# Kernel optimization log

Hardware: AMD Instinct MI355X
Metric: run time of the kernel (lower is better)

## Reference

```python
import jax, jax.numpy as jnp
import numpy as np

HIDDEN = 1152
N_HEADS = 4
N_KV = 1
HEAD_DIM = 256
EPS = 1e-6
B, S = 4, 2048
ROPE_THETA = 1000000.0


def _rms_norm(x, w):
    # x: [..., D] float32; Gemma-style (1 + w) scale
    xf = x.astype(jnp.float32)
    inv = jax.lax.rsqrt(jnp.mean(xf * xf, axis=-1, keepdims=True) + EPS)
    return (xf * inv * (1.0 + w.astype(jnp.float32))).astype(x.dtype)


def _apply_rope(x, cos, sin):
    # x: [B, H, S, D]; cos/sin: [S, D/2]
    d2 = x.shape[-1] // 2
    x1, x2 = x[..., :d2], x[..., d2:]
    cos = cos[None, None, :, :]
    sin = sin[None, None, :, :]
    xr = x1 * cos - x2 * sin
    xi = x1 * sin + x2 * cos
    return jnp.concatenate([xr, xi], axis=-1).astype(x.dtype)


def setup_inputs() -> dict:
    key = jax.random.key(0)
    k_h, k_qkv, k_qn, k_kn, k_o = jax.random.split(key, 5)
    hidden_states = jax.random.normal(k_h, (B, S, HIDDEN), dtype=jnp.float32)
    # causal additive mask [1,1,S,S]
    neg = jnp.finfo(jnp.float32).min
    causal = jnp.tril(jnp.ones((S, S), dtype=bool))
    attention_mask = jnp.where(causal, 0.0, neg)[None, None, :, :].astype(jnp.float32)
    # RoPE tables (complex freqs_cis split into cos/sin)
    inv_freq = 1.0 / (ROPE_THETA ** (np.arange(0, HEAD_DIM, 2, dtype=np.float32) / HEAD_DIM))
    ang = np.arange(S, dtype=np.float32)[:, None] * inv_freq[None, :]
    freqs_cos = jnp.asarray(np.cos(ang))
    freqs_sin = jnp.asarray(np.sin(ang))
    qkv_out = (N_HEADS + 2 * N_KV) * HEAD_DIM
    scale = HIDDEN ** -0.5
    w_qkv = jax.random.normal(k_qkv, (HIDDEN, qkv_out), dtype=jnp.float32) * scale
    w_o = jax.random.normal(k_o, (N_HEADS * HEAD_DIM, HIDDEN), dtype=jnp.float32) * (N_HEADS * HEAD_DIM) ** -0.5
    q_norm_w = jax.random.normal(k_qn, (HEAD_DIM,), dtype=jnp.float32) * 0.02
    k_norm_w = jax.random.normal(k_kn, (HEAD_DIM,), dtype=jnp.float32) * 0.02
    return {
        "hidden_states": hidden_states,
        "attention_mask": attention_mask,
        "freqs_cos": freqs_cos,
        "freqs_sin": freqs_sin,
        "w_qkv": w_qkv,
        "q_norm_w": q_norm_w,
        "k_norm_w": k_norm_w,
        "w_o": w_o,
    }


def reference(hidden_states, attention_mask, freqs_cos, freqs_sin, w_qkv, q_norm_w, k_norm_w, w_o):
    b, s, _ = hidden_states.shape
    groups = N_HEADS // N_KV
    scaling = HEAD_DIM ** -0.5

    qkv = jnp.einsum("bsh,ho->bso", hidden_states, w_qkv)
    q_end = N_HEADS * HEAD_DIM
    k_end = q_end + N_KV * HEAD_DIM
    q = qkv[:, :, :q_end].reshape(b, s, N_HEADS, HEAD_DIM).transpose(0, 2, 1, 3)
    k = qkv[:, :, q_end:k_end].reshape(b, s, N_KV, HEAD_DIM).transpose(0, 2, 1, 3)
    v = qkv[:, :, k_end:].reshape(b, s, N_KV, HEAD_DIM).transpose(0, 2, 1, 3)

    q = _rms_norm(q, q_norm_w)
    k = _rms_norm(k, k_norm_w)

    q = _apply_rope(q, freqs_cos, freqs_sin)
    k = _apply_rope(k, freqs_cos, freqs_sin)

    if groups > 1:
        k = jnp.repeat(k, groups, axis=1)  # [B, H, S, D]
        v = jnp.repeat(v, groups, axis=1)

    scores = jnp.einsum("bhqd,bhkd->bhqk", q * scaling, k)
    scores = scores + attention_mask.astype(jnp.float32)
    probs = jax.nn.softmax(scores.astype(jnp.float32), axis=-1).astype(q.dtype)

    attn = jnp.einsum("bhqk,bhkd->bhqd", probs, v)
    attn = attn.transpose(0, 2, 1, 3).reshape(b, s, N_HEADS * HEAD_DIM)
    return jnp.einsum("bsf,fh->bsh", attn, w_o)
```

## Files before the change

kernel.cpp:

```cpp
#include <hip/hip_runtime.h>

typedef _Float16 f16;
typedef _Float16 f16x8 __attribute__((ext_vector_type(8)));
typedef _Float16 f16x4 __attribute__((ext_vector_type(4)));
typedef float f32x4 __attribute__((ext_vector_type(4)));

#define NH 4
#define HD 256
#define BB 4
#define SS 2048
#define HID 1152
#define QKV_N 1536
#define ODIM (NH * HD)

#define QKV16_OFF 0L
#define HID16_OFF 25165824L
#define OBUF_OFF 0L
#define OPART_OFF 33554432L
#define QB_OFF 50331648L
#define KB_OFF 67108864L
#define VT_OFF 71303168L
#define WQKVT_OFF 75497472L
#define WOT_OFF 79036416L
#define ML_OFF 81395712L

#define GLL16(gp, lp)                                                      \
  __builtin_amdgcn_global_load_lds(                                       \
      (const __attribute__((address_space(1))) char*)(gp),                \
      (__attribute__((address_space(3))) char*)(lp), 16, 0, 0)

__global__ __launch_bounds__(256) void cvt_f32_to_f16(
    const float* __restrict__ s, f16* __restrict__ d, long n) {
  long i = ((long)blockIdx.x * 256 + threadIdx.x) * 8;
  long stride = (long)gridDim.x * 256 * 8;
  for (; i < n; i += stride) {
    float4 a = *(const float4*)(s + i);
    float4 b = *(const float4*)(s + i + 4);
    f16x8 h = {(f16)a.x, (f16)a.y, (f16)a.z, (f16)a.w,
               (f16)b.x, (f16)b.y, (f16)b.z, (f16)b.w};
    *(f16x8*)(d + i) = h;
  }
}

template <typename ST>
__global__ __launch_bounds__(256) void transpose_cvt(
    const ST* __restrict__ src, long src_ld, long src_bs,
    f16* __restrict__ dst, long dst_ld, long dst_bs) {
  __shared__ float tile[32][33];
  src += (long)blockIdx.z * src_bs;
  dst += (long)blockIdx.z * dst_bs;
  int r0 = blockIdx.y * 32, c0 = blockIdx.x * 32;
  int tc = threadIdx.x & 31, tr = threadIdx.x >> 5;
#pragma unroll
  for (int i = 0; i < 4; ++i)
    tile[tr + i * 8][tc] = (float)src[(long)(r0 + tr + i * 8) * src_ld + c0 + tc];
  __syncthreads();
#pragma unroll
  for (int i = 0; i < 4; ++i)
    dst[(long)(c0 + tr + i * 8) * dst_ld + r0 + tc] = (f16)tile[tc][tr + i * 8];
}

template <typename CT>
__global__ __launch_bounds__(256, 3) void gemm_f16(
    const f16* __restrict__ A, const f16* __restrict__ Bt,
    CT* __restrict__ C, int K, int N) {
  __shared__ f16 As[128][64];
  __shared__ f16 Bs[128][64];
  int tid = threadIdx.x, wave = tid >> 6, lane = tid & 63;
  int l16 = lane & 15, lhi = lane >> 4;
  int wm = (wave >> 1) * 64, wn = (wave & 1) * 64;
  long bm = (long)blockIdx.x * 128, bn = (long)blockIdx.y * 128;
  f32x4 acc[4][4] = {};

  int srow = wave * 32 + (lane >> 3);
  int scol = (lane & 7) * 8;
  const f16* Ag = A + (bm + srow) * (long)K + scol;
  const f16* Bg = Bt + (bn + srow) * (long)K + scol;

  for (int k0 = 0; k0 < K; k0 += 64) {
#pragma unroll
    for (int i = 0; i < 4; ++i)
      GLL16(Ag + k0 + (long)i * 8 * K, &As[wave * 32 + i * 8][0]);
#pragma unroll
    for (int i = 0; i < 4; ++i)
      GLL16(Bg + k0 + (long)i * 8 * K, &Bs[wave * 32 + i * 8][0]);
    __syncthreads();
#pragma unroll
    for (int kb = 0; kb < 2; ++kb) {
      f16x8 af[4], bf[4];
#pragma unroll
      for (int i = 0; i < 4; ++i)
        af[i] = *(const f16x8*)&As[wm + i * 16 + l16][kb * 32 + lhi * 8];
#pragma unroll
      for (int j = 0; j < 4; ++j)
        bf[j] = *(const f16x8*)&Bs[wn + j * 16 + l16][kb * 32 + lhi * 8];
#pragma unroll
      for (int i = 0; i < 4; ++i)
#pragma unroll
        for (int j = 0; j < 4; ++j)
          acc[i][j] =
              __builtin_amdgcn_mfma_f32_16x16x32_f16(bf[j], af[i], acc[i][j], 0, 0, 0);
    }
    __syncthreads();
  }

#pragma unroll
  for (int i = 0; i < 4; ++i) {
    long m = bm + wm + i * 16 + l16;
#pragma unroll
    for (int j = 0; j < 4; ++j) {
      long n = bn + wn + j * 16 + lhi * 4;
      if constexpr (sizeof(CT) == 2) {
        f16x4 h = {(f16)acc[i][j][0], (f16)acc[i][j][1], (f16)acc[i][j][2],
                   (f16)acc[i][j][3]};
        *(f16x4*)&C[m * N + n] = h;
      } else {
        *(f32x4*)&C[m * N + n] = acc[i][j];
      }
    }
  }
}

__device__ __forceinline__ void norm_rope_store(
    const f16* __restrict__ x, const float* __restrict__ w,
    const float* __restrict__ fc, const float* __restrict__ fs,
    f16* __restrict__ dst, float scale, int lane) {
  float x0 = (float)x[lane], x1 = (float)x[lane + 64];
  float x2 = (float)x[lane + 128], x3 = (float)x[lane + 192];
  float ss = x0 * x0 + x1 * x1 + x2 * x2 + x3 * x3;
#pragma unroll
  for (int m = 1; m < 64; m <<= 1) ss += __shfl_xor(ss, m, 64);
  float inv = rsqrtf(ss * (1.0f / 256.0f) + 1e-6f);
  x0 *= inv * (1.0f + w[lane]);
  x1 *= inv * (1.0f + w[lane + 64]);
  x2 *= inv * (1.0f + w[lane + 128]);
  x3 *= inv * (1.0f + w[lane + 192]);
  float c0 = fc[lane], s0 = fs[lane], c1 = fc[lane + 64], s1 = fs[lane + 64];
  dst[lane]       = (f16)((x0 * c0 - x2 * s0) * scale);
  dst[lane + 64]  = (f16)((x1 * c1 - x3 * s1) * scale);
  dst[lane + 128] = (f16)((x0 * s0 + x2 * c0) * scale);
  dst[lane + 192] = (f16)((x1 * s1 + x3 * c1) * scale);
}

__global__ __launch_bounds__(256) void qkv_post(
    const f16* __restrict__ qkv, const float* __restrict__ qnw,
    const float* __restrict__ knw, const float* __restrict__ fcos,
    const float* __restrict__ fsin, f16* __restrict__ Q, f16* __restrict__ Kb) {
  long row = blockIdx.x;
  int b = (int)(row >> 11), s = (int)(row & 2047);
  int wave = threadIdx.x >> 6, lane = threadIdx.x & 63;
  const f16* base = qkv + row * QKV_N;
  const float* fc = fcos + (long)s * 128;
  const float* fs = fsin + (long)s * 128;
  norm_rope_store(base + wave * HD, qnw, fc, fs,
                  Q + ((long)(b * NH + wave) * SS + s) * HD, 0.0625f, lane);
  if (wave == 0)
    norm_rope_store(base + NH * HD, knw, fc, fs, Kb + row * HD, 1.0f, lane);
}

__global__ __launch_bounds__(256, 3) void attn_fwd(
    const f16* __restrict__ Q, const f16* __restrict__ Kb,
    const f16* __restrict__ Vt, f16* __restrict__ O,
    f16* __restrict__ Opart, float2* __restrict__ ml) {
  __shared__ f16 Klds[32][264];
  __shared__ f16 Vlds[256][40];
  __shared__ f16 Plds[4][16][40];
  int it = blockIdx.x, h = blockIdx.y, b = blockIdx.z;
  int qb, t0, t1, pidx = 0;
  bool split;
  if (it < 16) {
    qb = it; t0 = 0; t1 = 2 * qb + 2; split = false;
  } else {
    int j = it - 16;
    qb = 16 + (j >> 1);
    int s = j & 1, half = qb + 1;
    t0 = s * half; t1 = t0 + half; split = true;
    pidx = (((b * NH + h) << 4) + (qb - 16)) * 2 + s;
  }
  int tid = threadIdx.x, wave = tid >> 6, lane = tid & 63;
  int l16 = lane & 15, lhi = lane >> 4;
  int q0 = qb * 64 + wave * 16;

  const f16* Kg = Kb + (long)b * SS * HD;
  const f16* Vg = Vt + (long)b * HD * SS;

  f16x8 qf[8];
  const f16* Qbase = Q + ((long)(b * NH + h) * SS + q0 + l16) * HD + lhi * 8;
#pragma unroll
  for (int kb = 0; kb < 8; ++kb) qf[kb] = *(const f16x8*)(Qbase + kb * 32);

  f32x4 o[16] = {};
  float m_i = -1e30f, l_i = 0.f;

  int kr = tid >> 5, kc = (tid & 31) * 8;
  int rv = tid >> 2, vc = (tid & 3) * 8;

  for (int t = t0; t < t1; ++t) {
    int kv0 = t * 32;
    __syncthreads();
#pragma unroll
    for (int i = 0; i < 4; ++i)
      *(uint4*)&Klds[kr + i * 8][kc] =
          *(const uint4*)(Kg + (long)(kv0 + kr + i * 8) * HD + kc);
#pragma unroll
    for (int i = 0; i < 4; ++i)
      *(uint4*)&Vlds[rv + i * 64][vc] =
          *(const uint4*)(Vg + (long)(rv + i * 64) * SS + kv0 + vc);
    __syncthreads();

    f32x4 sc[2] = {};
#pragma unroll
    for (int kb = 0; kb < 8; ++kb) {
#pragma unroll
      for (int cf = 0; cf < 2; ++cf) {
        f16x8 kf = *(const f16x8*)&Klds[cf * 16 + l16][kb * 32 + lhi * 8];
        sc[cf] = __builtin_amdgcn_mfma_f32_16x16x32_f16(kf, qf[kb], sc[cf], 0, 0, 0);
      }
    }

    float p[8];
    float mx = -1e30f;
    int qrow = q0 + l16;
    if (t >= 2 * qb) {
#pragma unroll
      for (int cf = 0; cf < 2; ++cf)
#pragma unroll
        for (int r = 0; r < 4; ++r) {
          int kv = kv0 + cf * 16 + lhi * 4 + r;
          float s = (kv <= qrow) ? sc[cf][r] : -1e30f;
          p[cf * 4 + r] = s;
          mx = fmaxf(mx, s);
        }
    } else {
#pragma unroll
      for (int i = 0; i < 8; ++i) {
        float s = sc[i >> 2][i & 3];
        p[i] = s;
        mx = fmaxf(mx, s);
      }
    }
    mx = fmaxf(mx, __shfl_xor(mx, 16));
    mx = fmaxf(mx, __shfl_xor(mx, 32));
    float mn = fmaxf(m_i, mx);
    float scl = __expf(m_i - mn);
    float rs = 0.f;
#pragma unroll
    for (int i = 0; i < 8; ++i) {
      p[i] = __expf(p[i] - mn);
      rs += p[i];
    }
    rs += __shfl_xor(rs, 16);
    rs += __shfl_xor(rs, 32);
    l_i = l_i * scl + rs;
    m_i = mn;

#pragma unroll
    for (int cf = 0; cf < 2; ++cf) {
      f16x4 hp = {(f16)p[cf * 4], (f16)p[cf * 4 + 1], (f16)p[cf * 4 + 2],
                  (f16)p[cf * 4 + 3]};
      *(f16x4*)&Plds[wave][l16][cf * 16 + lhi * 4] = hp;
    }

    float s0 = __shfl(scl, lhi * 4 + 0);
    float s1 = __shfl(scl, lhi * 4 + 1);
    float s2 = __shfl(scl, lhi * 4 + 2);
    float s3 = __shfl(scl, lhi * 4 + 3);
#pragma unroll
    for (int nf = 0; nf < 16; ++nf) {
      o[nf][0] *= s0;
      o[nf][1] *= s1;
      o[nf][2] *= s2;
      o[nf][3] *= s3;
    }

    f16x8 pa = *(const f16x8*)&Plds[wave][l16][lhi * 8];
#pragma unroll
    for (int nf = 0; nf < 16; ++nf) {
      f16x8 vf = *(const f16x8*)&Vlds[nf * 16 + l16][lhi * 8];
      o[nf] = __builtin_amdgcn_mfma_f32_16x16x32_f16(pa, vf, o[nf], 0, 0, 0);
    }
  }

  float inv = 1.0f / l_i;
  float i0 = __shfl(inv, lhi * 4 + 0);
  float i1 = __shfl(inv, lhi * 4 + 1);
  float i2 = __shfl(inv, lhi * 4 + 2);
  float i3 = __shfl(inv, lhi * 4 + 3);
  float ir[4] = {i0, i1, i2, i3};
  if (!split) {
#pragma unroll
    for (int r = 0; r < 4; ++r) {
      long srow = q0 + lhi * 4 + r;
      f16* Orow = O + ((long)b * SS + srow) * ODIM + h * HD + l16;
#pragma unroll
      for (int nf = 0; nf < 16; ++nf) Orow[nf * 16] = (f16)(o[nf][r] * ir[r]);
    }
  } else {
#pragma unroll
    for (int r = 0; r < 4; ++r) {
      int rloc = wave * 16 + lhi * 4 + r;
      f16* Prow = Opart + ((long)pidx * 64 + rloc) * HD + l16;
#pragma unroll
      for (int nf = 0; nf < 16; ++nf) Prow[nf * 16] = (f16)(o[nf][r] * ir[r]);
    }
    if (lane < 16) {
      float2 v; v.x = m_i; v.y = l_i;
      ml[(long)pidx * 64 + wave * 16 + lane] = v;
    }
  }
}

__global__ __launch_bounds__(256) void attn_combine(
    const f16* __restrict__ Opart, const float2* __restrict__ ml,
    f16* __restrict__ O) {
  int qx = blockIdx.x, h = blockIdx.y, b = blockIdx.z;
  int qb = 16 + qx;
  int p0 = (((b * NH + h) << 4) + qx) * 2;
  int tid = threadIdx.x;
  int r = tid >> 2, d0 = (tid & 3) * 64;
  float2 a = ml[(long)p0 * 64 + r];
  float2 c = ml[(long)(p0 + 1) * 64 + r];
  float M = fmaxf(a.x, c.x);
  float w0 = a.y * __expf(a.x - M), w1 = c.y * __expf(c.x - M);
  float invL = 1.0f / (w0 + w1);
  w0 *= invL; w1 *= invL;
  const f16* o0 = Opart + ((long)p0 * 64 + r) * HD + d0;
  const f16* o1 = Opart + ((long)(p0 + 1) * 64 + r) * HD + d0;
  f16* Orow = O + ((long)b * SS + qb * 64 + r) * ODIM + h * HD + d0;
#pragma unroll
  for (int i = 0; i < 8; ++i) {
    f16x8 x = *(const f16x8*)(o0 + i * 8);
    f16x8 y = *(const f16x8*)(o1 + i * 8);
    f16x8 z;
#pragma unroll
    for (int j = 0; j < 8; ++j)
      z[j] = (f16)(w0 * (float)x[j] + w1 * (float)y[j]);
    *(f16x8*)(Orow + i * 8) = z;
  }
}

extern "C" void kernel_launch(void* const* d_in, const int* in_sizes, int n_in,
                              void* d_out, int out_size, void* d_ws, size_t ws_size,
                              hipStream_t stream) {
  const float* hidden = (const float*)d_in[0];
  const float* fcos = (const float*)d_in[2];
  const float* fsin = (const float*)d_in[3];
  const float* wqkv = (const float*)d_in[4];
  const float* qnw = (const float*)d_in[5];
  const float* knw = (const float*)d_in[6];
  const float* wo = (const float*)d_in[7];
  float* out = (float*)d_out;

  char* ws = (char*)d_ws;
  f16* qkv16 = (f16*)(ws + QKV16_OFF);
  f16* hid16 = (f16*)(ws + HID16_OFF);
  f16* Obuf = (f16*)(ws + OBUF_OFF);
  f16* Opart = (f16*)(ws + OPART_OFF);
  f16* Qb = (f16*)(ws + QB_OFF);
  f16* Kb = (f16*)(ws + KB_OFF);
  f16* Vt = (f16*)(ws + VT_OFF);
  f16* wqkvt = (f16*)(ws + WQKVT_OFF);
  f16* wot = (f16*)(ws + WOT_OFF);
  float2* ml = (float2*)(ws + ML_OFF);

  cvt_f32_to_f16<<<2048, 256, 0, stream>>>(hidden, hid16, (long)BB * SS * HID);

  transpose_cvt<float><<<dim3(QKV_N / 32, HID / 32, 1), 256, 0, stream>>>(
      wqkv, QKV_N, 0, wqkvt, HID, 0);
  transpose_cvt<float><<<dim3(HID / 32, ODIM / 32, 1), 256, 0, stream>>>(
      wo, HID, 0, wot, ODIM, 0);

  gemm_f16<f16><<<dim3(BB * SS / 128, QKV_N / 128), 256, 0, stream>>>(
      hid16, wqkvt, qkv16, HID, QKV_N);

  qkv_post<<<dim3(BB * SS), 256, 0, stream>>>(qkv16, qnw, knw, fcos, fsin, Qb, Kb);

  transpose_cvt<f16><<<dim3(HD / 32, SS / 32, BB), 256, 0, stream>>>(
      qkv16 + 1280, QKV_N, (long)SS * QKV_N, Vt, SS, (long)HD * SS);

  attn_fwd<<<dim3(48, NH, BB), 256, 0, stream>>>(Qb, Kb, Vt, Obuf, Opart, ml);
  attn_combine<<<dim3(16, NH, BB), 256, 0, stream>>>(Opart, ml, Obuf);

  gemm_f16<float><<<dim3(BB * SS / 128, HID / 128), 256, 0, stream>>>(
      Obuf, wot, out, ODIM, HID);
}
```

Before: 237.0 us.

## Enlarge attention query tile to 128 rows with balanced causal pairing and K/V register prefetch

Measured after the change: 307.3 us. 29.7% more time.

```diff
diff --git a/kernel.cpp b/kernel.cpp
--- a/kernel.cpp
+++ b/kernel.cpp
@@ -158,154 +158,191 @@
     norm_rope_store(base + NH * HD, knw, fc, fs, Kb + row * HD, 1.0f, lane);
 }
 
-__global__ __launch_bounds__(256, 3) void attn_fwd(
+__global__ __launch_bounds__(256, 1) void attn_fwd(
     const f16* __restrict__ Q, const f16* __restrict__ Kb,
     const f16* __restrict__ Vt, f16* __restrict__ O,
     f16* __restrict__ Opart, float2* __restrict__ ml) {
   __shared__ f16 Klds[32][264];
   __shared__ f16 Vlds[256][40];
-  __shared__ f16 Plds[4][16][40];
+  __shared__ f16 Plds[4][32][40];
   int it = blockIdx.x, h = blockIdx.y, b = blockIdx.z;
-  int qb, t0, t1, pidx = 0;
-  bool split;
-  if (it < 16) {
-    qb = it; t0 = 0; t1 = 2 * qb + 2; split = false;
-  } else {
-    int j = it - 16;
-    qb = 16 + (j >> 1);
-    int s = j & 1, half = qb + 1;
-    t0 = s * half; t1 = t0 + half; split = true;
-    pidx = (((b * NH + h) << 4) + (qb - 16)) * 2 + s;
-  }
+  int pi = it >> 1, s = it & 1;
   int tid = threadIdx.x, wave = tid >> 6, lane = tid & 63;
   int l16 = lane & 15, lhi = lane >> 4;
-  int q0 = qb * 64 + wave * 16;
 
   const f16* Kg = Kb + (long)b * SS * HD;
   const f16* Vg = Vt + (long)b * HD * SS;
-
-  f16x8 qf[8];
-  const f16* Qbase = Q + ((long)(b * NH + h) * SS + q0 + l16) * HD + lhi * 8;
-#pragma unroll
-  for (int kb = 0; kb < 8; ++kb) qf[kb] = *(const f16x8*)(Qbase + kb * 32);
-
-  f32x4 o[16] = {};
-  float m_i = -1e30f, l_i = 0.f;
+  const f16* Qh = Q + (long)(b * NH + h) * SS * HD;
 
   int kr = tid >> 5, kc = (tid & 31) * 8;
   int rv = tid >> 2, vc = (tid & 3) * 8;
 
-  for (int t = t0; t < t1; ++t) {
-    int kv0 = t * 32;
-    __syncthreads();
-#pragma unroll
-    for (int i = 0; i < 4; ++i)
-      *(uint4*)&Klds[kr + i * 8][kc] =
-          *(const uint4*)(Kg + (long)(kv0 + kr + i * 8) * HD + kc);
-#pragma unroll
-    for (int i = 0; i < 4; ++i)
-      *(uint4*)&Vlds[rv + i * 64][vc] =
-          *(const uint4*)(Vg + (long)(rv + i * 64) * SS + kv0 + vc);
-    __syncthreads();
-
-    f32x4 sc[2] = {};
-#pragma unroll
-    for (int kb = 0; kb < 8; ++kb) {
-#pragma unroll
-      for (int cf = 0; cf < 2; ++cf) {
-        f16x8 kf = *(const f16x8*)&Klds[cf * 16 + l16][kb * 32 + lhi * 8];
-        sc[cf] = __builtin_amdgcn_mfma_f32_16x16x32_f16(kf, qf[kb], sc[cf], 0, 0, 0);
-      }
-    }
-
-    float p[8];
-    float mx = -1e30f;
-    int qrow = q0 + l16;
-    if (t >= 2 * qb) {
-#pragma unroll
-      for (int cf = 0; cf < 2; ++cf)
+  int nrun = (s == 0) ? 2 : 1;
+  for (int run = 0; run < nrun; ++run) {
+    int mb, t0, t1, slot = 0;
+    bool fin;
+    if (s == 0 && run == 0) {
+      mb = pi; t0 = 0; t1 = 4 * pi + 4; fin = true;
+    } else {
+      mb = 15 - pi; fin = false;
+      slot = ((b * NH + h) * 8 + pi) * 2 + s;
+      if (s == 0) { t0 = 0; t1 = 30 - 4 * pi; }
+      else        { t0 = 30 - 4 * pi; t1 = 64 - 4 * pi; }
+    }
+    int q0 = mb * 128 + wave * 32;
+
+    f16x8 qf[2][8];
+#pragma unroll
+    for (int g = 0; g < 2; ++g) {
+      const f16* Qb2 = Qh + (long)(q0 + g * 16 + l16) * HD + lhi * 8;
+#pragma unroll
+      for (int kb = 0; kb < 8; ++kb) qf[g][kb] = *(const f16x8*)(Qb2 + kb * 32);
+    }
+
+    f32x4 o[2][16] = {};
+    float m_i[2] = {-1e30f, -1e30f}, l_i[2] = {0.f, 0.f};
+
+    uint4 kreg[4], vreg[4];
+    {
+      long kv0 = (long)t0 * 32;
+#pragma unroll
+      for (int i = 0; i < 4; ++i)
+        kreg[i] = *(const uint4*)(Kg + (kv0 + kr + i * 8) * HD + kc);
+#pragma unroll
+      for (int i = 0; i < 4; ++i)
+        vreg[i] = *(const uint4*)(Vg + (long)(rv + i * 64) * SS + kv0 + vc);
+    }
+
+    for (int t = t0; t < t1; ++t) {
+      __syncthreads();
+#pragma unroll
+      for (int i = 0; i < 4; ++i) *(uint4*)&Klds[kr + i * 8][kc] = kreg[i];
+#pragma unroll
+      for (int i = 0; i < 4; ++i) *(uint4*)&Vlds[rv + i * 64][vc] = vreg[i];
+      if (t + 1 < t1) {
+        long kv0n = (long)(t + 1) * 32;
+#pragma unroll
+        for (int i = 0; i < 4; ++i)
+          kreg[i] = *(const uint4*)(Kg + (kv0n + kr + i * 8) * HD + kc);
+#pragma unroll
+        for (int i = 0; i < 4; ++i)
+          vreg[i] = *(const uint4*)(Vg + (long)(rv + i * 64) * SS + kv0n + vc);
+      }
+      __syncthreads();
+
+      int kv0 = t * 32;
+      f32x4 sc[2][2] = {};
+#pragma unroll
+      for (int kb = 0; kb < 8; ++kb) {
+#pragma unroll
+        for (int cf = 0; cf < 2; ++cf) {
+          f16x8 kf = *(const f16x8*)&Klds[cf * 16 + l16][kb * 32 + lhi * 8];
+          sc[0][cf] =
+              __builtin_amdgcn_mfma_f32_16x16x32_f16(kf, qf[0][kb], sc[0][cf], 0, 0, 0);
+          sc[1][cf] =
+              __builtin_amdgcn_mfma_f32_16x16x32_f16(kf, qf[1][kb], sc[1][cf], 0, 0, 0);
+        }
+      }
+
+#pragma unroll
+      for (int g = 0; g < 2; ++g) {
+        float p[8];
+        float mx = -1e30f;
+        int qrow = q0 + g * 16 + l16;
+        if (kv0 + 31 > q0 + g * 16) {
+#pragma unroll
+          for (int cf = 0; cf < 2; ++cf)
+#pragma unroll
+            for (int r = 0; r < 4; ++r) {
+              int kv = kv0 + cf * 16 + lhi * 4 + r;
+              float sv = (kv <= qrow) ? sc[g][cf][r] : -1e30f;
+              p[cf * 4 + r] = sv;
+              mx = fmaxf(mx, sv);
+            }
+        } else {
+#pragma unroll
+          for (int i = 0; i < 8; ++i) {
+            float sv = sc[g][i >> 2][i & 3];
+            p[i] = sv;
+            mx = fmaxf(mx, sv);
+          }
+        }
+        mx = fmaxf(mx, __shfl_xor(mx, 16));
+        mx = fmaxf(mx, __shfl_xor(mx, 32));
+        float mn = fmaxf(m_i[g], mx);
+        float scl = __expf(m_i[g] - mn);
+        float rs = 0.f;
+#pragma unroll
+        for (int i = 0; i < 8; ++i) {
+          p[i] = __expf(p[i] - mn);
+          rs += p[i];
+        }
+        rs += __shfl_xor(rs, 16);
+        rs += __shfl_xor(rs, 32);
+        l_i[g] = l_i[g] * scl + rs;
+        m_i[g] = mn;
+
+#pragma unroll
+        for (int cf = 0; cf < 2; ++cf) {
+          f16x4 hp = {(f16)p[cf * 4], (f16)p[cf * 4 + 1], (f16)p[cf * 4 + 2],
+                      (f16)p[cf * 4 + 3]};
+          *(f16x4*)&Plds[wave][g * 16 + l16][cf * 16 + lhi * 4] = hp;
+        }
+
+        float s0 = __shfl(scl, lhi * 4 + 0);
+        float s1 = __shfl(scl, lhi * 4 + 1);
+        float s2 = __shfl(scl, lhi * 4 + 2);
+        float s3 = __shfl(scl, lhi * 4 + 3);
+#pragma unroll
+        for (int nf = 0; nf < 16; ++nf) {
+          o[g][nf][0] *= s0;
+          o[g][nf][1] *= s1;
+          o[g][nf][2] *= s2;
+          o[g][nf][3] *= s3;
+        }
+      }
+
+      f16x8 pa0 = *(const f16x8*)&Plds[wave][l16][lhi * 8];
+      f16x8 pa1 = *(const f16x8*)&Plds[wave][16 + l16][lhi * 8];
+#pragma unroll
+      for (int nf = 0; nf < 16; ++nf) {
+        f16x8 vf = *(const f16x8*)&Vlds[nf * 16 + l16][lhi * 8];
+        o[0][nf] = __builtin_amdgcn_mfma_f32_16x16x32_f16(pa0, vf, o[0][nf], 0, 0, 0);
+        o[1][nf] = __builtin_amdgcn_mfma_f32_16x16x32_f16(pa1, vf, o[1][nf], 0, 0, 0);
+      }
+    }
+
+#pragma unroll
+    for (int g = 0; g < 2; ++g) {
+      float inv = 1.0f / l_i[g];
+      float i0 = __shfl(inv, lhi * 4 + 0);
+      float i1 = __shfl(inv, lhi * 4 + 1);
+      float i2 = __shfl(inv, lhi * 4 + 2);
+      float i3 = __shfl(inv, lhi * 4 + 3);
+      float ir[4] = {i0, i1, i2, i3};
+      if (fin) {
 #pragma unroll
         for (int r = 0; r < 4; ++r) {
-          int kv = kv0 + cf * 16 + lhi * 4 + r;
-          float s = (kv <= qrow) ? sc[cf][r] : -1e30f;
-          p[cf * 4 + r] = s;
-          mx = fmaxf(mx, s);
-        }
-    } else {
-#pragma unroll
-      for (int i = 0; i < 8; ++i) {
-        float s = sc[i >> 2][i & 3];
-        p[i] = s;
-        mx = fmaxf(mx, s);
-      }
-    }
-    mx = fmaxf(mx, __shfl_xor(mx, 16));
-    mx = fmaxf(mx, __shfl_xor(mx, 32));
-    float mn = fmaxf(m_i, mx);
-    float scl = __expf(m_i - mn);
-    float rs = 0.f;
-#pragma unroll
-    for (int i = 0; i < 8; ++i) {
-      p[i] = __expf(p[i] - mn);
-      rs += p[i];
-    }
-    rs += __shfl_xor(rs, 16);
-    rs += __shfl_xor(rs, 32);
-    l_i = l_i * scl + rs;
-    m_i = mn;
-
-#pragma unroll
-    for (int cf = 0; cf < 2; ++cf) {
-      f16x4 hp = {(f16)p[cf * 4], (f16)p[cf * 4 + 1], (f16)p[cf * 4 + 2],
-                  (f16)p[cf * 4 + 3]};
-      *(f16x4*)&Plds[wave][l16][cf * 16 + lhi * 4] = hp;
-    }
-
-    float s0 = __shfl(scl, lhi * 4 + 0);
-    float s1 = __shfl(scl, lhi * 4 + 1);
-    float s2 = __shfl(scl, lhi * 4 + 2);
-    float s3 = __shfl(scl, lhi * 4 + 3);
-#pragma unroll
-    for (int nf = 0; nf < 16; ++nf) {
-      o[nf][0] *= s0;
-      o[nf][1] *= s1;
-      o[nf][2] *= s2;
-      o[nf][3] *= s3;
-    }
-
-    f16x8 pa = *(const f16x8*)&Plds[wave][l16][lhi * 8];
-#pragma unroll
-    for (int nf = 0; nf < 16; ++nf) {
-      f16x8 vf = *(const f16x8*)&Vlds[nf * 16 + l16][lhi * 8];
-      o[nf] = __builtin_amdgcn_mfma_f32_16x16x32_f16(pa, vf, o[nf], 0, 0, 0);
-    }
-  }
-
-  float inv = 1.0f / l_i;
-  float i0 = __shfl(inv, lhi * 4 + 0);
-  float i1 = __shfl(inv, lhi * 4 + 1);
-  float i2 = __shfl(inv, lhi * 4 + 2);
-  float i3 = __shfl(inv, lhi * 4 + 3);
-  float ir[4] = {i0, i1, i2, i3};
-  if (!split) {
-#pragma unroll
-    for (int r = 0; r < 4; ++r) {
-      long srow = q0 + lhi * 4 + r;
-      f16* Orow = O + ((long)b * SS + srow) * ODIM + h * HD + l16;
-#pragma unroll
-      for (int nf = 0; nf < 16; ++nf) Orow[nf * 16] = (f16)(o[nf][r] * ir[r]);
-    }
-  } else {
-#pragma unroll
-    for (int r = 0; r < 4; ++r) {
-      int rloc = wave * 16 + lhi * 4 + r;
-      f16* Prow = Opart + ((long)pidx * 64 + rloc) * HD + l16;
-#pragma unroll
-      for (int nf = 0; nf < 16; ++nf) Prow[nf * 16] = (f16)(o[nf][r] * ir[r]);
-    }
-    if (lane < 16) {
-      float2 v; v.x = m_i; v.y = l_i;
-      ml[(long)pidx * 64 + wave * 16 + lane] = v;
+          long srow = q0 + g * 16 + lhi * 4 + r;
+          f16* Orow = O + ((long)b * SS + srow) * ODIM + h * HD + l16;
+#pragma unroll
+          for (int nf = 0; nf < 16; ++nf)
+            Orow[nf * 16] = (f16)(o[g][nf][r] * ir[r]);
+        }
+      } else {
+#pragma unroll
+        for (int r = 0; r < 4; ++r) {
+          int rloc = wave * 32 + g * 16 + lhi * 4 + r;
+          f16* Prow = Opart + ((long)slot * 128 + rloc) * HD + l16;
+#pragma unroll
+          for (int nf = 0; nf < 16; ++nf)
+            Prow[nf * 16] = (f16)(o[g][nf][r] * ir[r]);
+        }
+        if (lhi == 0) {
+          float2 v; v.x = m_i[g]; v.y = l_i[g];
+          ml[(long)slot * 128 + wave * 32 + g * 16 + l16] = v;
+        }
+      }
     }
   }
 }
@@ -313,22 +350,22 @@
 __global__ __launch_bounds__(256) void attn_combine(
     const f16* __restrict__ Opart, const float2* __restrict__ ml,
     f16* __restrict__ O) {
-  int qx = blockIdx.x, h = blockIdx.y, b = blockIdx.z;
-  int qb = 16 + qx;
-  int p0 = (((b * NH + h) << 4) + qx) * 2;
+  int pi = blockIdx.x, h = blockIdx.y, b = blockIdx.z;
+  int mb = 15 - pi;
+  int p0 = ((b * NH + h) * 8 + pi) * 2;
   int tid = threadIdx.x;
-  int r = tid >> 2, d0 = (tid & 3) * 64;
-  float2 a = ml[(long)p0 * 64 + r];
-  float2 c = ml[(long)(p0 + 1) * 64 + r];
+  int r = tid >> 1, d0 = (tid & 1) * 128;
+  float2 a = ml[(long)p0 * 128 + r];
+  float2 c = ml[(long)(p0 + 1) * 128 + r];
   float M = fmaxf(a.x, c.x);
   float w0 = a.y * __expf(a.x - M), w1 = c.y * __expf(c.x - M);
   float invL = 1.0f / (w0 + w1);
   w0 *= invL; w1 *= invL;
-  const f16* o0 = Opart + ((long)p0 * 64 + r) * HD + d0;
-  const f16* o1 = Opart + ((long)(p0 + 1) * 64 + r) * HD + d0;
-  f16* Orow = O + ((long)b * SS + qb * 64 + r) * ODIM + h * HD + d0;
-#pragma unroll
-  for (int i = 0; i < 8; ++i) {
+  const f16* o0 = Opart + ((long)p0 * 128 + r) * HD + d0;
+  const f16* o1 = Opart + ((long)(p0 + 1) * 128 + r) * HD + d0;
+  f16* Orow = O + ((long)b * SS + mb * 128 + r) * ODIM + h * HD + d0;
+#pragma unroll
+  for (int i = 0; i < 16; ++i) {
     f16x8 x = *(const f16x8*)(o0 + i * 8);
     f16x8 y = *(const f16x8*)(o1 + i * 8);
     f16x8 z;
@@ -378,8 +415,8 @@
   transpose_cvt<f16><<<dim3(HD / 32, SS / 32, BB), 256, 0, stream>>>(
       qkv16 + 1280, QKV_N, (long)SS * QKV_N, Vt, SS, (long)HD * SS);
 
-  attn_fwd<<<dim3(48, NH, BB), 256, 0, stream>>>(Qb, Kb, Vt, Obuf, Opart, ml);
-  attn_combine<<<dim3(16, NH, BB), 256, 0, stream>>>(Opart, ml, Obuf);
+  attn_fwd<<<dim3(16, NH, BB), 256, 0, stream>>>(Qb, Kb, Vt, Obuf, Opart, ml);
+  attn_combine<<<dim3(8, NH, BB), 256, 0, stream>>>(Opart, ml, Obuf);
 
   gemm_f16<float><<<dim3(BB * SS / 128, HID / 128), 256, 0, stream>>>(
       Obuf, wot, out, ODIM, HID);
```

## Load attention K/V tiles via direct global-to-LDS with XOR swizzle and setprio

Applied to the files above, without the earlier changes.

Result: slower. 253.7 us (+7.1%).

```diff
diff --git a/kernel.cpp b/kernel.cpp
--- a/kernel.cpp
+++ b/kernel.cpp
@@ -158,12 +158,12 @@
     norm_rope_store(base + NH * HD, knw, fc, fs, Kb + row * HD, 1.0f, lane);
 }
 
-__global__ __launch_bounds__(256, 3) void attn_fwd(
+__global__ __launch_bounds__(256, 4) void attn_fwd(
     const f16* __restrict__ Q, const f16* __restrict__ Kb,
     const f16* __restrict__ Vt, f16* __restrict__ O,
     f16* __restrict__ Opart, float2* __restrict__ ml) {
-  __shared__ f16 Klds[32][264];
-  __shared__ f16 Vlds[256][40];
+  __shared__ f16 Klds[32 * 256];
+  __shared__ f16 Vlds[256 * 32];
   __shared__ f16 Plds[4][16][40];
   int it = blockIdx.x, h = blockIdx.y, b = blockIdx.z;
   int qb, t0, t1, pidx = 0;
@@ -192,31 +192,49 @@
   f32x4 o[16] = {};
   float m_i = -1e30f, l_i = 0.f;
 
-  int kr = tid >> 5, kc = (tid & 31) * 8;
-  int rv = tid >> 2, vc = (tid & 3) * 8;
+  int l31 = lane & 31, lh5 = lane >> 5;
+  long koff[4];
+#pragma unroll
+  for (int i = 0; i < 4; ++i) {
+    int r = wave * 8 + 2 * i + lh5;
+    int csrc = (l31 * 16) ^ (((2 * i + lh5) & 7) << 4);
+    koff[i] = (long)r * HD + (csrc >> 1);
+  }
+  int lh2 = lane >> 2;
+  int vcsrc = ((lane & 3) * 16) ^ ((lh2 & 3) << 4);
+  long voff[4];
+#pragma unroll
+  for (int i = 0; i < 4; ++i)
+    voff[i] = (long)(wave * 64 + i * 16 + lh2) * SS + (vcsrc >> 1);
+
+  char* kldsb = (char*)Klds + wave * 4096;
+  char* vldsb = (char*)Vlds + wave * 4096;
+
+  int kx = (l16 & 7) << 4;
+  int vcol = (lhi * 16) ^ ((l16 & 3) << 4);
+  const char* krd = (const char*)Klds + l16 * 512;
+  const char* vrd = (const char*)Vlds + l16 * 64 + vcol;
 
   for (int t = t0; t < t1; ++t) {
-    int kv0 = t * 32;
+    long kv0 = (long)t * 32;
     __syncthreads();
 #pragma unroll
-    for (int i = 0; i < 4; ++i)
-      *(uint4*)&Klds[kr + i * 8][kc] =
-          *(const uint4*)(Kg + (long)(kv0 + kr + i * 8) * HD + kc);
-#pragma unroll
-    for (int i = 0; i < 4; ++i)
-      *(uint4*)&Vlds[rv + i * 64][vc] =
-          *(const uint4*)(Vg + (long)(rv + i * 64) * SS + kv0 + vc);
+    for (int i = 0; i < 4; ++i) GLL16(Kg + kv0 * HD + koff[i], kldsb + i * 1024);
+#pragma unroll
+    for (int i = 0; i < 4; ++i) GLL16(Vg + kv0 + voff[i], vldsb + i * 1024);
     __syncthreads();
 
     f32x4 sc[2] = {};
+    __builtin_amdgcn_s_setprio(1);
 #pragma unroll
     for (int kb = 0; kb < 8; ++kb) {
 #pragma unroll
       for (int cf = 0; cf < 2; ++cf) {
-        f16x8 kf = *(const f16x8*)&Klds[cf * 16 + l16][kb * 32 + lhi * 8];
+        f16x8 kf = *(const f16x8*)(krd + cf * 8192 + ((kb * 64 + lhi * 16) ^ kx));
         sc[cf] = __builtin_amdgcn_mfma_f32_16x16x32_f16(kf, qf[kb], sc[cf], 0, 0, 0);
       }
     }
+    __builtin_amdgcn_s_setprio(0);
 
     float p[8];
     float mx = -1e30f;
@@ -226,7 +244,7 @@
       for (int cf = 0; cf < 2; ++cf)
 #pragma unroll
         for (int r = 0; r < 4; ++r) {
-          int kv = kv0 + cf * 16 + lhi * 4 + r;
+          int kv = (int)kv0 + cf * 16 + lhi * 4 + r;
           float s = (kv <= qrow) ? sc[cf][r] : -1e30f;
           p[cf * 4 + r] = s;
           mx = fmaxf(mx, s);
@@ -274,11 +292,13 @@
     }
 
     f16x8 pa = *(const f16x8*)&Plds[wave][l16][lhi * 8];
+    __builtin_amdgcn_s_setprio(1);
 #pragma unroll
     for (int nf = 0; nf < 16; ++nf) {
-      f16x8 vf = *(const f16x8*)&Vlds[nf * 16 + l16][lhi * 8];
+      f16x8 vf = *(const f16x8*)(vrd + nf * 1024);
       o[nf] = __builtin_amdgcn_mfma_f32_16x16x32_f16(pa, vf, o[nf], 0, 0, 0);
     }
+    __builtin_amdgcn_s_setprio(0);
   }
 
   float inv = 1.0f / l_i;
```
